# Optimization experiments

Hardware: AMD Instinct MI355X
Metric: run time of the kernel (lower is better)

Reference implementation:

```python
import jax, jax.numpy as jnp
import numpy as np
import math

H = 32       # num query heads
HKV = 8      # num kv heads
D = 64       # head_dim
ROPE_BASE = 10000.0


def rotate_half(x):
    x1, x2 = x[..., : x.shape[-1] // 2], x[..., x.shape[-1] // 2 :]
    return jnp.concatenate((-x2, x1), axis=-1)


def rope_cos_sin(T, dim, dtype):
    inv_freq = 1.0 / (ROPE_BASE ** (jnp.arange(0, dim, 2, dtype=jnp.float32) / dim))
    pos = jnp.arange(T, dtype=jnp.float32)
    freqs = pos[:, None] * inv_freq[None, :]          # [T, dim/2]
    emb = jnp.concatenate((freqs, freqs), axis=-1)    # [T, dim]
    return jnp.cos(emb).astype(dtype), jnp.sin(emb).astype(dtype)


def setup_inputs() -> dict:
    key = jax.random.key(0)
    ks = jax.random.split(key, 6)
    B, T, C = 2, 2048, 2048
    x = jax.random.normal(ks[0], (B, T, C), dtype=jnp.float32)
    mask = jnp.triu(jnp.ones((T, T), dtype=jnp.float32), k=1)  # 1 above diagonal (masked)
    s = 1.0 / math.sqrt(C)
    wq = jax.random.normal(ks[1], (C, C), dtype=jnp.float32) * s
    wk = jax.random.normal(ks[2], (HKV * D, C), dtype=jnp.float32) * s
    wv = jax.random.normal(ks[3], (HKV * D, C), dtype=jnp.float32) * s
    wc = jax.random.normal(ks[4], (C, C), dtype=jnp.float32) * s
    return {"x": x, "mask": mask, "wq": wq, "wk": wk, "wv": wv, "wc": wc}


def reference(x, mask, wq, wk, wv, wc):
    B, T, C = x.shape
    n_rep = H // HKV
    # projections (Linear: x @ W^T)
    q = (x @ wq.T).reshape(B, T, H, D).transpose(0, 2, 1, 3)      # [B,H,T,D]
    k = (x @ wk.T).reshape(B, T, HKV, D).transpose(0, 2, 1, 3)    # [B,HKV,T,D]
    v = (x @ wv.T).reshape(B, T, HKV, D).transpose(0, 2, 1, 3)
    # RoPE
    cos, sin = rope_cos_sin(T, D, x.dtype)                        # [T,D]
    cos, sin = cos[None, None], sin[None, None]                   # [1,1,T,D]
    q = q * cos + rotate_half(q) * sin
    k = k * cos + rotate_half(k) * sin
    # GQA expand kv heads
    k = jnp.repeat(k, n_rep, axis=1)                              # [B,H,T,D]
    v = jnp.repeat(v, n_rep, axis=1)
    # attention
    scores = jnp.einsum('bhqd,bhkd->bhqk', q, k) / math.sqrt(D)
    scores = scores + mask * (-1e9)
    attn = jax.nn.softmax(scores, axis=-1)
    y = jnp.einsum('bhqk,bhkd->bhqd', attn, v)                    # [B,H,T,D]
    y = y.transpose(0, 2, 1, 3).reshape(B, T, C)
    return y @ wc.T
```

## Files before the change

### kernel.cpp

```cpp
#include <hip/hip_runtime.h>
#include <hip/hip_bf16.h>
#include <math.h>

typedef unsigned short u16;
typedef short s16x8 __attribute__((ext_vector_type(8)));
typedef u16 u16x4 __attribute__((ext_vector_type(4)));
typedef __bf16 bf16x8_t __attribute__((ext_vector_type(8)));
typedef float f32x4 __attribute__((ext_vector_type(4)));

#define DEVI static __device__ __forceinline__

static constexpr int Bn = 2, Tn = 2048, Cn = 2048, Hn = 32, HKVn = 8, Dn = 64;
static constexpr int NCOL = Cn + 2 * HKVn * Dn;
#define QSCALE 0.18033688011f
#define FMAXC 24.0f

#if __has_builtin(__builtin_amdgcn_exp2f)
#define EXP2(x) __builtin_amdgcn_exp2f(x)
#else
#define EXP2(x) exp2f(x)
#endif

DEVI u16 f2b(float f) {
  __hip_bfloat16 h = __float2bfloat16(f);
  return __builtin_bit_cast(u16, h);
}
DEVI float b2f(u16 u) {
  __hip_bfloat16 h = __builtin_bit_cast(__hip_bfloat16, u);
  return __bfloat162float(h);
}
DEVI bf16x8_t ld8(const u16* p) {
  s16x8 v = *reinterpret_cast<const s16x8*>(p);
  return __builtin_bit_cast(bf16x8_t, v);
}
DEVI f32x4 mfma16(bf16x8_t a, bf16x8_t b, f32x4 c) {
  return __builtin_amdgcn_mfma_f32_16x16x32_bf16(a, b, c, 0, 0, 0);
}
DEVI void async16(u16* lds_dst, const u16* gsrc) {
  __builtin_amdgcn_global_load_lds(
      (__attribute__((address_space(1))) void*)(gsrc),
      (__attribute__((address_space(3))) void*)(lds_dst), 16, 0, 0);
}

__global__ void cast_all(const float* __restrict__ x, const float* __restrict__ wq,
                         const float* __restrict__ wk, const float* __restrict__ wv,
                         const float* __restrict__ wc, u16* __restrict__ xb,
                         u16* __restrict__ wqkvb, u16* __restrict__ wcb,
                         float* __restrict__ cs, float* __restrict__ sn) {
  constexpr int NX4 = 2097152, NWQ4 = 1048576, NWK4 = 262144;
  constexpr int TOT = NX4 + NWQ4 + 2 * NWK4 + NWQ4;
  const int stride = gridDim.x * blockDim.x;
  const int tid0 = blockIdx.x * blockDim.x + threadIdx.x;
  for (int i = tid0; i < TOT; i += stride) {
    const float4* sv;
    u16x4* dv;
    if (i < NX4) {
      sv = (const float4*)x + i; dv = (u16x4*)xb + i;
    } else if (i < NX4 + NWQ4) {
      const int j = i - NX4;
      sv = (const float4*)wq + j; dv = (u16x4*)wqkvb + j;
    } else if (i < NX4 + NWQ4 + NWK4) {
      const int j = i - NX4 - NWQ4;
      sv = (const float4*)wk + j; dv = (u16x4*)wqkvb + NWQ4 + j;
    } else if (i < NX4 + NWQ4 + 2 * NWK4) {
      const int j = i - NX4 - NWQ4 - NWK4;
      sv = (const float4*)wv + j; dv = (u16x4*)wqkvb + NWQ4 + NWK4 + j;
    } else {
      const int j = i - NX4 - NWQ4 - 2 * NWK4;
      sv = (const float4*)wc + j; dv = (u16x4*)wcb + j;
    }
    const float4 v = *sv;
    u16x4 o = { f2b(v.x), f2b(v.y), f2b(v.z), f2b(v.w) };
    *dv = o;
  }
  if (tid0 < Tn * 32) {
    const int t = tid0 >> 5, d2 = tid0 & 31;
    const float inv = powf(10000.0f, -(float)d2 / 32.0f);
    const float fr = (float)t * inv;
    cs[tid0] = cosf(fr);
    sn[tid0] = sinf(fr);
  }
}

__global__ __launch_bounds__(512, 2)
void gemm_qkv_rope256(const u16* __restrict__ A, const u16* __restrict__ Bm,
                      const float* __restrict__ cs, const float* __restrict__ sn,
                      u16* __restrict__ qo, u16* __restrict__ ko,
                      u16* __restrict__ vo, int K) {
  __shared__ u16 lds[2][20480];
  const int tid = threadIdx.x;
  const int mb = blockIdx.x * 128, nb = blockIdx.y * 192;
  const int lane = tid & 63, lr = lane & 15, lg = lane >> 4;
  const int w = tid >> 6, wm = w >> 2, wn = w & 3;
  const int nk = K >> 6;

  auto stage = [&](int buf, int kt) {
#pragma unroll
    for (int h = 0; h < 5; ++h) {
      if (h < 2) {
        const int s = h * 512 + tid;
        const int row = s >> 3;
        const int c = (s & 7) ^ (row & 7);
        async16(&lds[buf][s * 8], A + (size_t)(mb + row) * K + kt * 64 + c * 8);
      } else {
        const int s = (h - 2) * 512 + tid;
        const int row = s >> 3;
        const int c = (s & 7) ^ (row & 7);
        async16(&lds[buf][8192 + s * 8],
                Bm + (size_t)(nb + row) * K + kt * 64 + c * 8);
      }
    }
  };

  f32x4 acc[4][3] = {};
  stage(0, 0);
  stage(1, 1);

  const int rsw = lr & 7;
  for (int kt = 0; kt < nk; ++kt) {
    if (kt + 1 < nk) asm volatile("s_waitcnt vmcnt(5)" ::: "memory");
    else             asm volatile("s_waitcnt vmcnt(0)" ::: "memory");
    asm volatile("s_barrier" ::: "memory");
    const u16* base = lds[kt & 1];
    bf16x8_t bfr[3][2];
#pragma unroll
    for (int n = 0; n < 3; ++n)
#pragma unroll
      for (int ks = 0; ks < 2; ++ks)
        bfr[n][ks] = ld8(base + 8192 + (wn * 48 + n * 16 + lr) * 64 +
                         (((ks * 4 + lg) ^ rsw) * 8));
#pragma unroll
    for (int p = 0; p < 2; ++p) {
      bf16x8_t af[2][2];
#pragma unroll
      for (int mi = 0; mi < 2; ++mi)
#pragma unroll
        for (int ks = 0; ks < 2; ++ks)
          af[mi][ks] = ld8(base + (wm * 64 + (p * 2 + mi) * 16 + lr) * 64 +
                           (((ks * 4 + lg) ^ rsw) * 8));
      __builtin_amdgcn_s_setprio(1);
#pragma unroll
      for (int mi = 0; mi < 2; ++mi)
#pragma unroll
        for (int n = 0; n < 3; ++n) {
          acc[p * 2 + mi][n] = mfma16(af[mi][0], bfr[n][0], acc[p * 2 + mi][n]);
          acc[p * 2 + mi][n] = mfma16(af[mi][1], bfr[n][1], acc[p * 2 + mi][n]);
        }
      __builtin_amdgcn_s_setprio(0);
    }
    asm volatile("s_barrier" ::: "memory");
    if (kt + 2 < nk) stage(kt & 1, kt + 2);
  }
  __syncthreads();

  u16* tile = &lds[0][0];
#pragma unroll
  for (int m = 0; m < 4; ++m)
#pragma unroll
    for (int n = 0; n < 3; ++n) {
      const int fragcol = nb + wn * 48 + n * 16;
      if (fragcol >= Cn + 512) {
        const int cc = fragcol + lr - Cn - 512;
        const int d = cc & 63, h = cc >> 6;
        const int row0 = mb + wm * 64 + m * 16 + lg * 4;
        const int b = row0 >> 11, t0 = row0 & 2047;
        u16x4 pk = { f2b(acc[m][n][0]), f2b(acc[m][n][1]),
                     f2b(acc[m][n][2]), f2b(acc[m][n][3]) };
        *reinterpret_cast<u16x4*>(
            vo + (((size_t)b * HKVn + h) * Dn + d) * Tn + t0) = pk;
      } else {
        const int colc = wn * 48 + n * 16 + lr;
#pragma unroll
        for (int r = 0; r < 4; ++r) {
          const int row = wm * 64 + m * 16 + lg * 4 + r;
          tile[row * 192 + (((colc >> 3) ^ (row & 7)) << 3) + (colc & 7)] =
              f2b(acc[m][n][r]);
        }
      }
    }
  if (nb >= Cn + 512) return;
  __syncthreads();

#pragma unroll
  for (int it = 0; it < 6; ++it) {
    const int unit = it * 512 + tid;
    const int tl = unit / 24;
    const int ch = unit - tl * 24;
    const int gcol = nb + ch * 8;
    if (gcol >= Cn + 512) continue;
    const int c = ch & 7;
    const int sw = tl & 7;
    const s16x8 v0 = *reinterpret_cast<const s16x8*>(
        tile + tl * 192 + ((ch ^ sw) << 3));
    const s16x8 v1 = *reinterpret_cast<const s16x8*>(
        tile + tl * 192 + (((ch ^ 4) ^ sw) << 3));
    const int grow = mb + tl, b = grow >> 11, t = grow & 2047;
    const float4 c0 = *reinterpret_cast<const float4*>(cs + t * 32 + (c & 3) * 8);
    const float4 c1 = *reinterpret_cast<const float4*>(cs + t * 32 + (c & 3) * 8 + 4);
    const float4 s0 = *reinterpret_cast<const float4*>(sn + t * 32 + (c & 3) * 8);
    const float4 s1 = *reinterpret_cast<const float4*>(sn + t * 32 + (c & 3) * 8 + 4);
    const float cf[8] = { c0.x, c0.y, c0.z, c0.w, c1.x, c1.y, c1.z, c1.w };
    const float sf[8] = { s0.x, s0.y, s0.z, s0.w, s1.x, s1.y, s1.z, s1.w };
    const float sgn = (c < 4) ? -1.f : 1.f;
    const bool isQ = (gcol < Cn);
    const float scale = isQ ? QSCALE : 1.f;
    u16 outv[8];
#pragma unroll
    for (int e = 0; e < 8; ++e) {
      const float a0 = b2f((u16)v0[e]);
      const float a1 = b2f((u16)v1[e]);
      outv[e] = f2b((a0 * cf[e] + sgn * a1 * sf[e]) * scale);
    }
    u16* dst;
    if (isQ) {
      const int h = gcol >> 6;
      dst = qo + (((size_t)b * Hn + h) * Tn + t) * Dn + c * 8;
    } else {
      const int h = (gcol - Cn) >> 6;
      dst = ko + (((size_t)b * HKVn + h) * Tn + t) * Dn + c * 8;
    }
    *reinterpret_cast<s16x8*>(dst) = *reinterpret_cast<const s16x8*>(outv);
  }
}

__global__ __launch_bounds__(512, 2)
void gemm_proj256(const u16* __restrict__ A, const u16* __restrict__ Bm,
                  float* __restrict__ Cm, int N, int K) {
  __shared__ u16 lds[2][16384];
  const int tid = threadIdx.x;
  const int mb = blockIdx.x * 128, nb = blockIdx.y * 128;
  const int lane = tid & 63, lr = lane & 15, lg = lane >> 4;
  const int w = tid >> 6, wm = w >> 2, wn = w & 3;
  const int nk = K >> 6;

  auto stage = [&](int buf, int kt) {
#pragma unroll
    for (int h = 0; h < 4; ++h) {
      if (h < 2) {
        const int s = h * 512 + tid;
        const int row = s >> 3;
        const int c = (s & 7) ^ (row & 7);
        async16(&lds[buf][s * 8], A + (size_t)(mb + row) * K + kt * 64 + c * 8);
      } else {
        const int s = (h - 2) * 512 + tid;
        const int row = s >> 3;
        const int c = (s & 7) ^ (row & 7);
        async16(&lds[buf][8192 + s * 8],
                Bm + (size_t)(nb + row) * K + kt * 64 + c * 8);
      }
    }
  };

  f32x4 acc[4][2] = {};
  stage(0, 0);
  stage(1, 1);

  const int rsw = lr & 7;
  for (int kt = 0; kt < nk; ++kt) {
    if (kt + 1 < nk) asm volatile("s_waitcnt vmcnt(4)" ::: "memory");
    else             asm volatile("s_waitcnt vmcnt(0)" ::: "memory");
    asm volatile("s_barrier" ::: "memory");
    const u16* base = lds[kt & 1];
    bf16x8_t bfr[2][2];
#pragma unroll
    for (int n = 0; n < 2; ++n)
#pragma unroll
      for (int ks = 0; ks < 2; ++ks)
        bfr[n][ks] = ld8(base + 8192 + (wn * 32 + n * 16 + lr) * 64 +
                         (((ks * 4 + lg) ^ rsw) * 8));
#pragma unroll
    for (int p = 0; p < 2; ++p) {
      bf16x8_t af[2][2];
#pragma unroll
      for (int mi = 0; mi < 2; ++mi)
#pragma unroll
        for (int ks = 0; ks < 2; ++ks)
          af[mi][ks] = ld8(base + (wm * 64 + (p * 2 + mi) * 16 + lr) * 64 +
                           (((ks * 4 + lg) ^ rsw) * 8));
      __builtin_amdgcn_s_setprio(1);
#pragma unroll
      for (int mi = 0; mi < 2; ++mi)
#pragma unroll
        for (int n = 0; n < 2; ++n) {
          acc[p * 2 + mi][n] = mfma16(af[mi][0], bfr[n][0], acc[p * 2 + mi][n]);
          acc[p * 2 + mi][n] = mfma16(af[mi][1], bfr[n][1], acc[p * 2 + mi][n]);
        }
      __builtin_amdgcn_s_setprio(0);
    }
    asm volatile("s_barrier" ::: "memory");
    if (kt + 2 < nk) stage(kt & 1, kt + 2);
  }

#pragma unroll
  for (int m = 0; m < 4; ++m)
#pragma unroll
    for (int n = 0; n < 2; ++n) {
      const int col = nb + wn * 32 + n * 16 + lr;
#pragma unroll
      for (int r = 0; r < 4; ++r) {
        const int row = mb + wm * 64 + m * 16 + lg * 4 + r;
        Cm[(size_t)row * N + col] = acc[m][n][r];
      }
    }
}

__global__ __launch_bounds__(256, 2)
void flash_kernel(const u16* __restrict__ q, const u16* __restrict__ k,
                  const u16* __restrict__ vt, u16* __restrict__ y) {
  __shared__ u16 kbuf[2][4096];
  __shared__ u16 vbuf[2][4096];
  __shared__ u16 plds[4][2048];
  const int tid = threadIdx.x;
  const int w = tid >> 6, lane = tid & 63, lr = lane & 15, lg = lane >> 4;
  const int bx = blockIdx.x;
  const int xb = 15 - (bx >> 6);
  const int bh = bx & 63;
  const int b = bh >> 5, h = bh & 31, hkv = h >> 2;
  const u16* kb_base = k + ((size_t)(b * HKVn + hkv)) * Tn * Dn;
  const u16* vb_base = vt + ((size_t)(b * HKVn + hkv)) * Dn * Tn;

  const int qb0 = xb * 128;
  const int ntiles = 2 * xb + 2;
  const int qw0 = qb0 + w * 32;
  const int qrow0 = qw0 + lr;

  const int slot0 = w * 128 + lane;
  const int slot1 = slot0 + 64;
  const int r0 = slot0 >> 3, c0 = (slot0 & 7) ^ (r0 & 7);
  const int r1 = slot1 >> 3, c1 = (slot1 & 7) ^ (r1 & 7);
  const u16* ksrc0 = kb_base + r0 * Dn + c0 * 8;
  const u16* ksrc1 = kb_base + r1 * Dn + c1 * 8;
  const u16* vsrc0 = vb_base + r0 * Tn + c0 * 8;
  const u16* vsrc1 = vb_base + r1 * Tn + c1 * 8;

  int off[4][2];
#pragma unroll
  for (int i = 0; i < 4; ++i)
#pragma unroll
    for (int ks = 0; ks < 2; ++ks)
      off[i][ks] = (i * 16 + lr) * 64 + (((ks * 4 + lg) ^ (lr & 7)) * 8);

  u16* pw = plds[w];
  const int swz = (lr & 7) * 8;

  auto stageKV = [&](int buf, int t) {
    const int ko = t * 64 * Dn;
    const int vo_ = t * 64;
    async16(&kbuf[buf][slot0 * 8], ksrc0 + ko);
    async16(&kbuf[buf][slot1 * 8], ksrc1 + ko);
    async16(&vbuf[buf][slot0 * 8], vsrc0 + vo_);
    async16(&vbuf[buf][slot1 * 8], vsrc1 + vo_);
  };

  bf16x8_t aq[2][2];
  {
    const u16* qp = q + (((size_t)(b * Hn + h)) * Tn + qw0 + lr) * Dn + lg * 8;
    aq[0][0] = ld8(qp);
    aq[0][1] = ld8(qp + 32);
    aq[1][0] = ld8(qp + 16 * Dn);
    aq[1][1] = ld8(qp + 16 * Dn + 32);
  }

  f32x4 acc[2][4] = {};
  float lsum[2] = { 0.f, 0.f };
  const f32x4 cinit = { -FMAXC, -FMAXC, -FMAXC, -FMAXC };

  stageKV(0, 0);
  stageKV(1, 1);

  for (int kb = 0; kb < ntiles; ++kb) {
    if (kb + 1 < ntiles) asm volatile("s_waitcnt vmcnt(4)" ::: "memory");
    else                 asm volatile("s_waitcnt vmcnt(0)" ::: "memory");
    asm volatile("s_barrier" ::: "memory");
    const int kp0 = kb * 64;
    if (kp0 <= qw0 + 31) {
      const u16* kl = kbuf[kb & 1];
      const u16* vl = vbuf[kb & 1];
      f32x4 sc[2][4] = { { cinit, cinit, cinit, cinit },
                         { cinit, cinit, cinit, cinit } };
#pragma unroll
      for (int ks = 0; ks < 2; ++ks) {
        bf16x8_t kf0 = ld8(kl + off[0][ks]);
        bf16x8_t kf1 = ld8(kl + off[1][ks]);
        bf16x8_t kf2 = ld8(kl + off[2][ks]);
        bf16x8_t kf3 = ld8(kl + off[3][ks]);
#pragma unroll
        for (int rt = 0; rt < 2; ++rt) {
          sc[rt][0] = mfma16(kf0, aq[rt][ks], sc[rt][0]);
          sc[rt][1] = mfma16(kf1, aq[rt][ks], sc[rt][1]);
          sc[rt][2] = mfma16(kf2, aq[rt][ks], sc[rt][2]);
          sc[rt][3] = mfma16(kf3, aq[rt][ks], sc[rt][3]);
        }
      }
#pragma unroll
      for (int rt = 0; rt < 2; ++rt) {
        const int qrow = qrow0 + rt * 16;
        const bool needmask = (kp0 + 63) > (qw0 + rt * 16);
        if (needmask) {
#pragma unroll
          for (int kt = 0; kt < 4; ++kt) {
            const int kbase = kp0 + kt * 16 + lg * 4;
#pragma unroll
            for (int jj = 0; jj < 4; ++jj)
              if ((kbase + jj) > qrow) sc[rt][kt][jj] = -3e38f;
          }
        }
        float tsum[4];
#pragma unroll
        for (int kt = 0; kt < 4; ++kt) {
#pragma unroll
          for (int jj = 0; jj < 4; ++jj)
            sc[rt][kt][jj] = EXP2(sc[rt][kt][jj]);
          tsum[kt] = (sc[rt][kt][0] + sc[rt][kt][1]) +
                     (sc[rt][kt][2] + sc[rt][kt][3]);
        }
        lsum[rt] += (tsum[0] + tsum[1]) + (tsum[2] + tsum[3]);
#pragma unroll
        for (int kt = 0; kt < 4; ++kt) {
          u16x4 pk = { f2b(sc[rt][kt][0]), f2b(sc[rt][kt][1]),
                       f2b(sc[rt][kt][2]), f2b(sc[rt][kt][3]) };
          *reinterpret_cast<u16x4*>(
              pw + (rt * 16 + lr) * 64 + ((kt * 16 + lg * 4) ^ swz)) = pk;
        }
      }
#pragma unroll
      for (int ks = 0; ks < 2; ++ks) {
        bf16x8_t pb0 = ld8(pw + lr * 64 + ((ks * 32 + lg * 8) ^ swz));
        bf16x8_t pb1 = ld8(pw + (16 + lr) * 64 + ((ks * 32 + lg * 8) ^ swz));
#pragma unroll
        for (int dt = 0; dt < 4; ++dt) {
          bf16x8_t vf = ld8(vl + off[dt][ks]);
          acc[0][dt] = mfma16(vf, pb0, acc[0][dt]);
          acc[1][dt] = mfma16(vf, pb1, acc[1][dt]);
        }
      }
    }
    asm volatile("s_barrier" ::: "memory");
    if (kb + 2 < ntiles) stageKV(kb & 1, kb + 2);
  }

#pragma unroll
  for (int rt = 0; rt < 2; ++rt) {
    lsum[rt] += __shfl_xor(lsum[rt], 16, 64);
    lsum[rt] += __shfl_xor(lsum[rt], 32, 64);
  }

  u16* scratch = &kbuf[0][0] + w * 2048;
#pragma unroll
  for (int rt = 0; rt < 2; ++rt) {
    float inv = 1.f / lsum[rt];
#pragma unroll
    for (int dt = 0; dt < 4; ++dt) {
      u16x4 pk = { f2b(acc[rt][dt][0] * inv), f2b(acc[rt][dt][1] * inv),
                   f2b(acc[rt][dt][2] * inv), f2b(acc[rt][dt][3] * inv) };
      *reinterpret_cast<u16x4*>(
          scratch + (rt * 16 + lr) * 64 + ((dt * 16 + lg * 4) ^ swz)) = pk;
    }
  }
#pragma unroll
  for (int it = 0; it < 4; ++it) {
    const int row = it * 8 + (lane >> 3);
    const int col = (lane & 7) * 8;
    s16x8 vv = *reinterpret_cast<const s16x8*>(
        scratch + row * 64 + (col ^ ((row & 7) * 8)));
    *reinterpret_cast<s16x8*>(
        y + ((size_t)b * Tn + qb0 + w * 32 + row) * Cn + h * 64 + col) = vv;
  }
}

extern "C" void kernel_launch(void* const* d_in, const int* in_sizes, int n_in,
                              void* d_out, int out_size, void* d_ws, size_t ws_size,
                              hipStream_t stream) {
  const float* x  = (const float*)d_in[0];
  const float* wq = (const float*)d_in[2];
  const float* wk = (const float*)d_in[3];
  const float* wv = (const float*)d_in[4];
  const float* wc = (const float*)d_in[5];
  float* out = (float*)d_out;
  char* ws = (char*)d_ws;

  const size_t NX   = (size_t)Bn * Tn * Cn;
  const size_t NWQ  = (size_t)Cn * Cn;
  const size_t NWK  = (size_t)HKVn * Dn * Cn;
  const size_t NQ   = (size_t)Bn * Hn * Tn * Dn;
  const size_t NKV  = (size_t)Bn * HKVn * Tn * Dn;

  size_t off = 0;
  u16* xb    = (u16*)(ws + off); off += NX * 2;
  u16* wqkvb = (u16*)(ws + off); off += (NWQ + 2 * NWK) * 2;
  u16* wcb   = (u16*)(ws + off); off += NWQ * 2;
  u16* qr    = (u16*)(ws + off); off += NQ * 2;
  u16* kr    = (u16*)(ws + off); off += NKV * 2;
  u16* vt    = (u16*)(ws + off); off += NKV * 2;
  float* cs  = (float*)(ws + off); off += (size_t)Tn * 32 * 4;
  float* sn  = (float*)(ws + off); off += (size_t)Tn * 32 * 4;

  u16* y = xb;

  cast_all<<<2048, 256, 0, stream>>>(x, wq, wk, wv, wc, xb, wqkvb, wcb, cs, sn);

  gemm_qkv_rope256<<<dim3(32, 16), 512, 0, stream>>>(
      xb, wqkvb, cs, sn, qr, kr, vt, Cn);

  flash_kernel<<<dim3(1024), 256, 0, stream>>>(qr, kr, vt, y);

  gemm_proj256<<<dim3(32, 16), 512, 0, stream>>>(
      y, wcb, out, Cn, Cn);

  (void)in_sizes; (void)n_in; (void)out_size; (void)ws_size;
}
```

Baseline: 153.7 us.

## Retile QKV+RoPE GEMM to 128x128 tiles with 32-wide K steps

Changes the fused QKV projection + RoPE GEMM from 128x192 tiles with 64-wide K stages to 128x128 tiles with 32-wide K stages, growing the grid from 32x16 to 32x24 blocks. LDS use drops sharply and each tile now maps cleanly to Q, K or V heads, which simplifies the epilogue and removes the per-column branch. The aim is more blocks in flight for better CU occupancy and load balance. The cost is less data reuse per K step, twice as many barriers and waits, and fewer MFMAs per barrier to hide latency.

```diff
diff --git a/kernel.cpp b/kernel.cpp
--- a/kernel.cpp
+++ b/kernel.cpp
@@ -87,80 +87,61 @@
                       const float* __restrict__ cs, const float* __restrict__ sn,
                       u16* __restrict__ qo, u16* __restrict__ ko,
                       u16* __restrict__ vo, int K) {
-  __shared__ u16 lds[2][20480];
+  __shared__ u16 lds[2][8192];
   const int tid = threadIdx.x;
-  const int mb = blockIdx.x * 128, nb = blockIdx.y * 192;
+  const int mb = blockIdx.x * 128, nb = blockIdx.y * 128;
   const int lane = tid & 63, lr = lane & 15, lg = lane >> 4;
   const int w = tid >> 6, wm = w >> 2, wn = w & 3;
-  const int nk = K >> 6;
+  const int nk = K >> 5;
+
+  const int srow = tid >> 2;
+  const int scol = ((tid & 3) ^ ((tid >> 3) & 3));
+  const u16* asrc = A + (size_t)(mb + srow) * K + scol * 8;
+  const u16* bsrc = Bm + (size_t)(nb + srow) * K + scol * 8;
 
   auto stage = [&](int buf, int kt) {
-#pragma unroll
-    for (int h = 0; h < 5; ++h) {
-      if (h < 2) {
-        const int s = h * 512 + tid;
-        const int row = s >> 3;
-        const int c = (s & 7) ^ (row & 7);
-        async16(&lds[buf][s * 8], A + (size_t)(mb + row) * K + kt * 64 + c * 8);
-      } else {
-        const int s = (h - 2) * 512 + tid;
-        const int row = s >> 3;
-        const int c = (s & 7) ^ (row & 7);
-        async16(&lds[buf][8192 + s * 8],
-                Bm + (size_t)(nb + row) * K + kt * 64 + c * 8);
-      }
-    }
+    async16(&lds[buf][tid * 8], asrc + kt * 32);
+    async16(&lds[buf][4096 + tid * 8], bsrc + kt * 32);
   };
 
-  f32x4 acc[4][3] = {};
+  f32x4 acc[4][2] = {};
   stage(0, 0);
   stage(1, 1);
 
-  const int rsw = lr & 7;
+  const int rsw = (lr >> 1) & 3;
   for (int kt = 0; kt < nk; ++kt) {
-    if (kt + 1 < nk) asm volatile("s_waitcnt vmcnt(5)" ::: "memory");
+    if (kt + 1 < nk) asm volatile("s_waitcnt vmcnt(2)" ::: "memory");
     else             asm volatile("s_waitcnt vmcnt(0)" ::: "memory");
     asm volatile("s_barrier" ::: "memory");
     const u16* base = lds[kt & 1];
-    bf16x8_t bfr[3][2];
-#pragma unroll
-    for (int n = 0; n < 3; ++n)
-#pragma unroll
-      for (int ks = 0; ks < 2; ++ks)
-        bfr[n][ks] = ld8(base + 8192 + (wn * 48 + n * 16 + lr) * 64 +
-                         (((ks * 4 + lg) ^ rsw) * 8));
-#pragma unroll
-    for (int p = 0; p < 2; ++p) {
-      bf16x8_t af[2][2];
-#pragma unroll
-      for (int mi = 0; mi < 2; ++mi)
-#pragma unroll
-        for (int ks = 0; ks < 2; ++ks)
-          af[mi][ks] = ld8(base + (wm * 64 + (p * 2 + mi) * 16 + lr) * 64 +
-                           (((ks * 4 + lg) ^ rsw) * 8));
-      __builtin_amdgcn_s_setprio(1);
-#pragma unroll
-      for (int mi = 0; mi < 2; ++mi)
-#pragma unroll
-        for (int n = 0; n < 3; ++n) {
-          acc[p * 2 + mi][n] = mfma16(af[mi][0], bfr[n][0], acc[p * 2 + mi][n]);
-          acc[p * 2 + mi][n] = mfma16(af[mi][1], bfr[n][1], acc[p * 2 + mi][n]);
-        }
-      __builtin_amdgcn_s_setprio(0);
-    }
+    bf16x8_t bfr[2];
+#pragma unroll
+    for (int n = 0; n < 2; ++n)
+      bfr[n] = ld8(base + 4096 + (wn * 32 + n * 16 + lr) * 32 +
+                   ((lg ^ rsw) * 8));
+    bf16x8_t af[4];
+#pragma unroll
+    for (int m = 0; m < 4; ++m)
+      af[m] = ld8(base + (wm * 64 + m * 16 + lr) * 32 + ((lg ^ rsw) * 8));
+    __builtin_amdgcn_s_setprio(1);
+#pragma unroll
+    for (int m = 0; m < 4; ++m)
+#pragma unroll
+      for (int n = 0; n < 2; ++n)
+        acc[m][n] = mfma16(af[m], bfr[n], acc[m][n]);
+    __builtin_amdgcn_s_setprio(0);
     asm volatile("s_barrier" ::: "memory");
     if (kt + 2 < nk) stage(kt & 1, kt + 2);
   }
   __syncthreads();
 
-  u16* tile = &lds[0][0];
-#pragma unroll
-  for (int m = 0; m < 4; ++m)
-#pragma unroll
-    for (int n = 0; n < 3; ++n) {
-      const int fragcol = nb + wn * 48 + n * 16;
-      if (fragcol >= Cn + 512) {
-        const int cc = fragcol + lr - Cn - 512;
+  if (nb >= Cn + 512) {
+#pragma unroll
+    for (int m = 0; m < 4; ++m)
+#pragma unroll
+      for (int n = 0; n < 2; ++n) {
+        const int col = nb + wn * 32 + n * 16 + lr;
+        const int cc = col - Cn - 512;
         const int d = cc & 63, h = cc >> 6;
         const int row0 = mb + wm * 64 + m * 16 + lg * 4;
         const int b = row0 >> 11, t0 = row0 & 2047;
@@ -168,32 +149,38 @@
                      f2b(acc[m][n][2]), f2b(acc[m][n][3]) };
         *reinterpret_cast<u16x4*>(
             vo + (((size_t)b * HKVn + h) * Dn + d) * Tn + t0) = pk;
-      } else {
-        const int colc = wn * 48 + n * 16 + lr;
-#pragma unroll
-        for (int r = 0; r < 4; ++r) {
-          const int row = wm * 64 + m * 16 + lg * 4 + r;
-          tile[row * 192 + (((colc >> 3) ^ (row & 7)) << 3) + (colc & 7)] =
-              f2b(acc[m][n][r]);
-        }
-      }
-    }
-  if (nb >= Cn + 512) return;
+      }
+    return;
+  }
+
+  u16* tile = &lds[0][0];
+#pragma unroll
+  for (int m = 0; m < 4; ++m)
+#pragma unroll
+    for (int n = 0; n < 2; ++n) {
+      const int colc = wn * 32 + n * 16 + lr;
+#pragma unroll
+      for (int r = 0; r < 4; ++r) {
+        const int row = wm * 64 + m * 16 + lg * 4 + r;
+        tile[row * 128 + (((colc >> 3) ^ (row & 15)) << 3) + (colc & 7)] =
+            f2b(acc[m][n][r]);
+      }
+    }
   __syncthreads();
 
-#pragma unroll
-  for (int it = 0; it < 6; ++it) {
+  const bool isQ = (nb < Cn);
+#pragma unroll
+  for (int it = 0; it < 4; ++it) {
     const int unit = it * 512 + tid;
-    const int tl = unit / 24;
-    const int ch = unit - tl * 24;
-    const int gcol = nb + ch * 8;
-    if (gcol >= Cn + 512) continue;
+    const int tl = unit >> 4;
+    const int ch = unit & 15;
+    const int head = ch >> 3;
     const int c = ch & 7;
-    const int sw = tl & 7;
+    const int sw = tl & 15;
     const s16x8 v0 = *reinterpret_cast<const s16x8*>(
-        tile + tl * 192 + ((ch ^ sw) << 3));
+        tile + tl * 128 + ((ch ^ sw) << 3));
     const s16x8 v1 = *reinterpret_cast<const s16x8*>(
-        tile + tl * 192 + (((ch ^ 4) ^ sw) << 3));
+        tile + tl * 128 + (((ch ^ 4) ^ sw) << 3));
     const int grow = mb + tl, b = grow >> 11, t = grow & 2047;
     const float4 c0 = *reinterpret_cast<const float4*>(cs + t * 32 + (c & 3) * 8);
     const float4 c1 = *reinterpret_cast<const float4*>(cs + t * 32 + (c & 3) * 8 + 4);
@@ -202,7 +189,6 @@
     const float cf[8] = { c0.x, c0.y, c0.z, c0.w, c1.x, c1.y, c1.z, c1.w };
     const float sf[8] = { s0.x, s0.y, s0.z, s0.w, s1.x, s1.y, s1.z, s1.w };
     const float sgn = (c < 4) ? -1.f : 1.f;
-    const bool isQ = (gcol < Cn);
     const float scale = isQ ? QSCALE : 1.f;
     u16 outv[8];
 #pragma unroll
@@ -213,10 +199,10 @@
     }
     u16* dst;
     if (isQ) {
-      const int h = gcol >> 6;
+      const int h = (nb >> 6) + head;
       dst = qo + (((size_t)b * Hn + h) * Tn + t) * Dn + c * 8;
     } else {
-      const int h = (gcol - Cn) >> 6;
+      const int h = ((nb - Cn) >> 6) + head;
       dst = ko + (((size_t)b * HKVn + h) * Tn + t) * Dn + c * 8;
     }
     *reinterpret_cast<s16x8*>(dst) = *reinterpret_cast<const s16x8*>(outv);
@@ -499,7 +485,7 @@
 
   cast_all<<<2048, 256, 0, stream>>>(x, wq, wk, wv, wc, xb, wqkvb, wcb, cs, sn);
 
-  gemm_qkv_rope256<<<dim3(32, 16), 512, 0, stream>>>(
+  gemm_qkv_rope256<<<dim3(32, 24), 512, 0, stream>>>(
       xb, wqkvb, cs, sn, qr, kr, vt, Cn);
 
   flash_kernel<<<dim3(1024), 256, 0, stream>>>(qr, kr, vt, y);
```

New measurement: 167.5 us. 1.09x slower.

## Double the flash-attention KV tile to 128 keys per barrier stage

Applied to the files above, without the earlier changes.

Each stage now loads 128 keys of K and V into shared memory instead of 64. The stage is processed as two 64-key halves, and the V layout is re-swizzled to a 128-wide row. This halves the number of barrier/waitcnt synchronisation points and async-load rounds per block. The cost is twice the LDS footprint (64KB for K/V double buffers plus P scratch), which may reduce occupancy below the two blocks per CU the launch bounds target, and loads that are partly masked at the causal edge.

```diff
diff --git a/kernel.cpp b/kernel.cpp
--- a/kernel.cpp
+++ b/kernel.cpp
@@ -307,8 +307,8 @@
 __global__ __launch_bounds__(256, 2)
 void flash_kernel(const u16* __restrict__ q, const u16* __restrict__ k,
                   const u16* __restrict__ vt, u16* __restrict__ y) {
-  __shared__ u16 kbuf[2][4096];
-  __shared__ u16 vbuf[2][4096];
+  __shared__ u16 kbuf[2][8192];
+  __shared__ u16 vbuf[2][8192];
   __shared__ u16 plds[4][2048];
   const int tid = threadIdx.x;
   const int w = tid >> 6, lane = tid & 63, lr = lane & 15, lg = lane >> 4;
@@ -320,18 +320,23 @@
   const u16* vb_base = vt + ((size_t)(b * HKVn + hkv)) * Dn * Tn;
 
   const int qb0 = xb * 128;
-  const int ntiles = 2 * xb + 2;
+  const int ntiles = xb + 1;
   const int qw0 = qb0 + w * 32;
   const int qrow0 = qw0 + lr;
 
-  const int slot0 = w * 128 + lane;
-  const int slot1 = slot0 + 64;
-  const int r0 = slot0 >> 3, c0 = (slot0 & 7) ^ (r0 & 7);
-  const int r1 = slot1 >> 3, c1 = (slot1 & 7) ^ (r1 & 7);
-  const u16* ksrc0 = kb_base + r0 * Dn + c0 * 8;
-  const u16* ksrc1 = kb_base + r1 * Dn + c1 * 8;
-  const u16* vsrc0 = vb_base + r0 * Tn + c0 * 8;
-  const u16* vsrc1 = vb_base + r1 * Tn + c1 * 8;
+  int kslot[4], vslot[4];
+  const u16* ksrc[4];
+  const u16* vsrc[4];
+#pragma unroll
+  for (int i = 0; i < 4; ++i) {
+    const int s = i * 256 + tid;
+    kslot[i] = s;
+    const int kr = s >> 3, kc = (s & 7) ^ (kr & 7);
+    ksrc[i] = kb_base + kr * Dn + kc * 8;
+    vslot[i] = s;
+    const int vr = s >> 4, vc = (s & 15) ^ (vr & 15);
+    vsrc[i] = vb_base + vr * Tn + vc * 8;
+  }
 
   int off[4][2];
 #pragma unroll
@@ -344,12 +349,13 @@
   const int swz = (lr & 7) * 8;
 
   auto stageKV = [&](int buf, int t) {
-    const int ko = t * 64 * Dn;
-    const int vo_ = t * 64;
-    async16(&kbuf[buf][slot0 * 8], ksrc0 + ko);
-    async16(&kbuf[buf][slot1 * 8], ksrc1 + ko);
-    async16(&vbuf[buf][slot0 * 8], vsrc0 + vo_);
-    async16(&vbuf[buf][slot1 * 8], vsrc1 + vo_);
+    const int ko = t * 128 * Dn;
+    const int vo_ = t * 128;
+#pragma unroll
+    for (int i = 0; i < 4; ++i) {
+      async16(&kbuf[buf][kslot[i] * 8], ksrc[i] + ko);
+      async16(&vbuf[buf][vslot[i] * 8], vsrc[i] + vo_);
+    }
   };
 
   bf16x8_t aq[2][2];
@@ -369,21 +375,24 @@
   stageKV(1, 1);
 
   for (int kb = 0; kb < ntiles; ++kb) {
-    if (kb + 1 < ntiles) asm volatile("s_waitcnt vmcnt(4)" ::: "memory");
+    if (kb + 1 < ntiles) asm volatile("s_waitcnt vmcnt(8)" ::: "memory");
     else                 asm volatile("s_waitcnt vmcnt(0)" ::: "memory");
     asm volatile("s_barrier" ::: "memory");
-    const int kp0 = kb * 64;
-    if (kp0 <= qw0 + 31) {
-      const u16* kl = kbuf[kb & 1];
-      const u16* vl = vbuf[kb & 1];
+    const u16* kl = kbuf[kb & 1];
+    const u16* vl = vbuf[kb & 1];
+#pragma unroll
+    for (int hf = 0; hf < 2; ++hf) {
+      const int kp0 = kb * 128 + hf * 64;
+      if (kp0 > qw0 + 31) continue;
+      const u16* klh = kl + hf * 4096;
       f32x4 sc[2][4] = { { cinit, cinit, cinit, cinit },
                          { cinit, cinit, cinit, cinit } };
 #pragma unroll
       for (int ks = 0; ks < 2; ++ks) {
-        bf16x8_t kf0 = ld8(kl + off[0][ks]);
-        bf16x8_t kf1 = ld8(kl + off[1][ks]);
-        bf16x8_t kf2 = ld8(kl + off[2][ks]);
-        bf16x8_t kf3 = ld8(kl + off[3][ks]);
+        bf16x8_t kf0 = ld8(klh + off[0][ks]);
+        bf16x8_t kf1 = ld8(klh + off[1][ks]);
+        bf16x8_t kf2 = ld8(klh + off[2][ks]);
+        bf16x8_t kf3 = ld8(klh + off[3][ks]);
 #pragma unroll
         for (int rt = 0; rt < 2; ++rt) {
           sc[rt][0] = mfma16(kf0, aq[rt][ks], sc[rt][0]);
@@ -429,7 +438,8 @@
         bf16x8_t pb1 = ld8(pw + (16 + lr) * 64 + ((ks * 32 + lg * 8) ^ swz));
 #pragma unroll
         for (int dt = 0; dt < 4; ++dt) {
-          bf16x8_t vf = ld8(vl + off[dt][ks]);
+          bf16x8_t vf = ld8(vl + (dt * 16 + lr) * 128 +
+                            (((hf * 8 + ks * 4 + lg) ^ lr) * 8));
           acc[0][dt] = mfma16(vf, pb0, acc[0][dt]);
           acc[1][dt] = mfma16(vf, pb1, acc[1][dt]);
         }
```

New measurement: 156.5 us. About the same (+1.8%).
